# Optimization experiments

Measured on AMD Instinct MI355X. Metric: run time of the kernel, lower is better.

## Reference

```python
import jax, jax.numpy as jnp
import numpy as np

# ---- constants matching the original module's globals ----
H = 16          # self.h: number of bit levels; self.n = h per the source
TP = 8          # self.tp: parallel coordinate channels
N_K = 2         # random masks per flipped bit
T = 512         # T_train: tokens per block
N_TRNBR = 128   # neighbor count
K_VOCAB = 128   # sampled vocab count
N_VOCAB = 50257 # full vocab size V for sampled softmax correction
D = 256         # embedding dim
RATIO_COS = 1.0
RATIO_CRO = 0.1
C_CNC = 2 * H * N_K + 1  # candidate locations per token = 65


def setup_inputs() -> dict:
    key = jax.random.key(0)
    ks = jax.random.split(key, 8)
    n = H  # code: self.n = h
    sta_loc = jax.random.randint(ks[0], (T, TP), 1 - n, n, dtype=jnp.int32)
    nei_loc = jax.random.randint(ks[1], (T, N_TRNBR, TP), 1 - n, n, dtype=jnp.int32)
    voc_loc = jax.random.randint(ks[2], (T, K_VOCAB, TP), 1 - n, n, dtype=jnp.int32)
    sta_emb = jax.random.normal(ks[3], (T, D), dtype=jnp.float32)
    nei_emb = jax.random.normal(ks[4], (T, N_TRNBR, D), dtype=jnp.float32)
    voc_emb = jax.random.normal(ks[5], (T, K_VOCAB, D), dtype=jnp.float32)
    # raw random numbers for generate_random_masks: randint(0, self.n)
    rand_masks = jax.random.randint(ks[6], (T, H, N_K, TP), 0, n, dtype=jnp.int32)
    # converge mode: mask is all ones (generate_mask with converge=True)
    mask = jnp.ones((T, N_TRNBR), dtype=bool)
    return {"sta_loc": sta_loc, "nei_loc": nei_loc, "voc_loc": voc_loc,
            "sta_emb": sta_emb, "nei_emb": nei_emb, "voc_emb": voc_emb,
            "rand_masks": rand_masks, "mask": mask}


def _cos_similarity(c1, c2):
    # sign product: (+1 if >=0 else -1) for each operand
    sg = ((2 * (c1 >= 0).astype(jnp.int32) - 1) *
          (2 * (c2 >= 0).astype(jnp.int32) - 1)).astype(jnp.float32)
    x = ((jnp.abs(c1) ^ jnp.abs(c2)) + 1).astype(jnp.float32)
    # torch.frexp exponent of v>=1 equals floor(log2(v)) + 1
    expo = jnp.floor(jnp.log2(x)) + 1.0
    return sg * (1.0 - expo / H)


def _connection(sta_loc, rand_masks):
    bits = jnp.arange(H, dtype=jnp.int32)
    flip_masks = (1 << bits)                          # [H]
    flipped = sta_loc[:, None, :] ^ flip_masks[None, :, None]  # [T,H,TP]
    # note operator precedence in source: rn & (2**i - 1)
    rm = rand_masks & (flip_masks - 1)[None, :, None, None]    # [T,H,N_K,TP]
    res = (flipped[:, :, None, :] ^ rm).reshape(sta_loc.shape[0], H * N_K, TP)
    return jnp.concatenate([res, sta_loc[:, None, :], -res], axis=1)  # [T,C,TP]


def _normalize(x):
    return x / jnp.maximum(jnp.linalg.norm(x, axis=-1, keepdims=True), 1e-12)


def reference(sta_loc, nei_loc, voc_loc, sta_emb, nei_emb, voc_emb, rand_masks, mask):
    cnc_loc = _connection(sta_loc, rand_masks)          # [T, C, TP]
    lth = mask.sum(axis=1).astype(jnp.float32) + 1e-12  # [T]

    # euclidean-space cosine targets: [T, N_trnbr]
    eu_cos_val = jnp.einsum('td,tnd->tn', _normalize(sta_emb), _normalize(nei_emb))
    # use_eu_norm == True branch: ||sta|| * ||voc|| -> [T, K_vocab]
    eu_cro_nrm = (jnp.linalg.norm(sta_emb, axis=-1, keepdims=True) *
                  jnp.linalg.norm(voc_emb, axis=-1))

    pos_loc = jnp.concatenate([nei_loc, voc_loc], axis=1)           # [T, P, TP]
    cos_sta_pos = _cos_similarity(sta_loc[:, None, :], pos_loc)     # [T, P, TP]
    cos_sta_pos_sum = cos_sta_pos.sum(axis=-1)                      # [T, P]
    cos_cnc_pos = _cos_similarity(cnc_loc[:, None, :, :], pos_loc[:, :, None, :])  # [T,P,C,TP]
    ct_val = (cos_sta_pos_sum[:, :, None, None]
              - cos_sta_pos[:, :, None, :] + cos_cnc_pos) / TP      # [T,P,C,TP]

    # cosine-matching loss over neighbors
    eu = eu_cos_val[:, :, None, None]                               # [T,N,1,1]
    loss_cos = ((ct_val[:, :N_TRNBR] - eu) ** 2 * jnp.abs(eu)
                * mask[:, :, None, None].astype(jnp.float32))
    loss_cos = loss_cos.sum(axis=1) / lth[:, None, None]            # [T, C, TP]

    # sampled softmax CE (uniform proposal), positive class at vocab index 0
    z = ct_val[:, N_TRNBR:] * eu_cro_nrm[:, :, None, None]          # [T, K, C, TP]
    corr = jnp.where(jnp.arange(K_VOCAB) == 0, 0.0,
                     jnp.log(N_VOCAB / K_VOCAB)).astype(jnp.float32)
    zc = z + corr[None, :, None, None]
    loss_cro = jax.scipy.special.logsumexp(zc, axis=1) - zc[:, 0]   # [T, C, TP]

    loss_tot = RATIO_COS * loss_cos + RATIO_CRO * loss_cro

    # get_best_loc with cur_portion=1.0, cur_tp=tp -> pure argmin selection
    idx = jnp.argmin(loss_tot, axis=1)                              # [T, TP]
    gather = lambda a: jnp.take_along_axis(a, idx[:, None, :], axis=1)[:, 0]
    selected_locs = gather(cnc_loc)                                 # [T, TP]
    real_loss_cos = gather(loss_cos).mean(axis=-1)                  # [T]
    real_loss_cro = gather(loss_cro).mean(axis=-1)
    real_loss_tot = gather(loss_tot).mean(axis=-1)
    return selected_locs, real_loss_cos, real_loss_cro, real_loss_tot
```

## Files before the change

kernel.cpp:

```cpp
#include <hip/hip_runtime.h>
#include <math.h>

#define T_DIM 512
#define TP 8
#define NC 65
#define NJ 128
#define BLOCK 576
#define LOG2E 1.4426950408889634f
#define LN2   0.6931471805599453f
#define CORR_L2 8.617045f

__device__ __forceinline__ float i2f(int x) { return __int_as_float(x); }
__device__ __forceinline__ int   f2i(float x) { return __float_as_int(x); }

__device__ __forceinline__ int cand_v(int c, int sta, const int* s_rand, int p) {
    if (c == 32) return sta;
    const int cc = (c < 32) ? c : (c - 33);
    const int h = cc >> 1;
    const int r = (sta ^ (1 << h)) ^ (s_rand[cc * TP + p] & ((1 << h) - 1));
    return (c < 32) ? r : -r;
}

#define COS_STEP(va, vs, X, acc) do {                                   \
    const int _x = (va) ^ (X).x;                                        \
    const float _u8 = fmaf((float)__clz(_x + 1), 0.0078125f, -0.125f);  \
    const float _d = i2f(f2i(_u8) ^ ((vs) ^ (X).y)) + i2f((X).z);       \
    (acc) = fmaf(_d * _d, i2f((X).w), (acc));                           \
} while (0)

#define CRO_Z(va, vs, X) ({                                             \
    const int _x = (va) ^ (X).x;                                        \
    const float _u0 = fmaf((float)__clz(_x + 1), 0.0625f, -1.0f);       \
    const float _u = i2f(f2i(_u0) ^ ((vs) ^ (X).y));                    \
    fmaf(_u, i2f((X).w), i2f((X).z));                                   \
})

__device__ __forceinline__ float cos_body1(int va, int vs, const int4* pc) {
    float a0 = 0.f, a1 = 0.f;
    #pragma unroll 2
    for (int j = 0; j < NJ; j += 2) {
        const int4 x = pc[j * 8];
        const int4 y = pc[(j + 1) * 8];
        COS_STEP(va, vs, x, a0);
        COS_STEP(va, vs, y, a1);
    }
    return (a0 + a1) * 0.0078125f;
}

__device__ __forceinline__ void cos_body2(int vaA, int vsA, int vaB, int vsB,
                                          const int4* pc, float* oA, float* oB) {
    float a0 = 0.f, a1 = 0.f, b0 = 0.f, b1 = 0.f;
    #pragma unroll 2
    for (int j = 0; j < NJ; j += 2) {
        const int4 x = pc[j * 8];
        const int4 y = pc[(j + 1) * 8];
        COS_STEP(vaA, vsA, x, a0);
        COS_STEP(vaB, vsB, x, b0);
        COS_STEP(vaA, vsA, y, a1);
        COS_STEP(vaB, vsB, y, b1);
    }
    *oA = (a0 + a1) * 0.0078125f;
    *oB = (b0 + b1) * 0.0078125f;
}

__device__ __forceinline__ float cro_body1(int va, int vs, const int4* pc, float M) {
    const int4 x0 = pc[0];
    const float z0 = CRO_Z(va, vs, x0) - M;
    float s0 = __builtin_amdgcn_exp2f(z0);
    const int4 x1 = pc[8];
    float s1 = __builtin_amdgcn_exp2f(CRO_Z(va, vs, x1) - M);
    #pragma unroll 2
    for (int k = 2; k < NJ; k += 2) {
        const int4 x = pc[k * 8];
        const int4 y = pc[(k + 1) * 8];
        s0 += __builtin_amdgcn_exp2f(CRO_Z(va, vs, x) - M);
        s1 += __builtin_amdgcn_exp2f(CRO_Z(va, vs, y) - M);
    }
    const float S = fmaxf(s0 + s1, 1e-38f);
    return (__builtin_amdgcn_logf(S) - z0) * LN2;
}

__device__ __forceinline__ void cro_body2(int vaA, int vsA, int vaB, int vsB,
                                          const int4* pc, float M, float* oA, float* oB) {
    const int4 x0 = pc[0];
    const float zA0 = CRO_Z(vaA, vsA, x0) - M;
    const float zB0 = CRO_Z(vaB, vsB, x0) - M;
    float sA0 = __builtin_amdgcn_exp2f(zA0);
    float sB0 = __builtin_amdgcn_exp2f(zB0);
    const int4 x1 = pc[8];
    float sA1 = __builtin_amdgcn_exp2f(CRO_Z(vaA, vsA, x1) - M);
    float sB1 = __builtin_amdgcn_exp2f(CRO_Z(vaB, vsB, x1) - M);
    #pragma unroll 2
    for (int k = 2; k < NJ; k += 2) {
        const int4 x = pc[k * 8];
        const int4 y = pc[(k + 1) * 8];
        sA0 += __builtin_amdgcn_exp2f(CRO_Z(vaA, vsA, x) - M);
        sB0 += __builtin_amdgcn_exp2f(CRO_Z(vaB, vsB, x) - M);
        sA1 += __builtin_amdgcn_exp2f(CRO_Z(vaA, vsA, y) - M);
        sB1 += __builtin_amdgcn_exp2f(CRO_Z(vaB, vsB, y) - M);
    }
    const float SA = fmaxf(sA0 + sA1, 1e-38f);
    const float SB = fmaxf(sB0 + sB1, 1e-38f);
    *oA = (__builtin_amdgcn_logf(SA) - zA0) * LN2;
    *oB = (__builtin_amdgcn_logf(SB) - zB0) * LN2;
}

__global__ __launch_bounds__(BLOCK, 5) void cg_fused(
    const int* __restrict__ sta_loc,
    const int* __restrict__ nei_loc,
    const int* __restrict__ voc_loc,
    const float* __restrict__ sta_emb,
    const float* __restrict__ nei_emb,
    const float* __restrict__ voc_emb,
    const int* __restrict__ rand_masks,
    float* __restrict__ out)
{
    const int t = blockIdx.x;
    const int tid = threadIdx.x;

    __shared__ int4  s_pc4[2][NJ * TP];
    __shared__ float s_cspT[2][TP * 132];
    __shared__ float s_css[2][NJ];
    __shared__ float s_w[2][NJ];
    __shared__ float s_dot[NJ];
    __shared__ float s_nn[2][NJ];
    __shared__ float s_lcos[NC * TP], s_lcro[NC * TP];
    __shared__ float s_Mpart[9 * 8];
    __shared__ float s_ss;
    __shared__ int   s_sta[TP];
    __shared__ int   s_rand[256];

    if (tid < 256) s_rand[tid] = rand_masks[t * 256 + tid];

    if (tid < 512) {
        const int g = tid >> 2, sub = tid & 3;
        const float4* sp = (const float4*)(sta_emb + (size_t)t * 256);
        const float4* np = (const float4*)(nei_emb + ((size_t)t * NJ + g) * 256);
        const float4* vp = (const float4*)(voc_emb + ((size_t)t * NJ + g) * 256);
        float dd = 0.f, nnn = 0.f, nnv = 0.f, ss = 0.f;
        #pragma unroll 4
        for (int i = 0; i < 16; ++i) {
            const int i4 = sub + 4 * i;
            const float4 a = sp[i4];
            const float4 b = np[i4];
            const float4 c = vp[i4];
            dd  += a.x * b.x + a.y * b.y + a.z * b.z + a.w * b.w;
            nnn += b.x * b.x + b.y * b.y + b.z * b.z + b.w * b.w;
            nnv += c.x * c.x + c.y * c.y + c.z * c.z + c.w * c.w;
            if (g == 0) ss += a.x * a.x + a.y * a.y + a.z * a.z + a.w * a.w;
        }
        dd  += __shfl_xor(dd, 1);  dd  += __shfl_xor(dd, 2);
        nnn += __shfl_xor(nnn, 1); nnn += __shfl_xor(nnn, 2);
        nnv += __shfl_xor(nnv, 1); nnv += __shfl_xor(nnv, 2);
        if (g == 0) { ss += __shfl_xor(ss, 1); ss += __shfl_xor(ss, 2); }
        if (sub == 0) {
            s_dot[g] = dd; s_nn[0][g] = nnn; s_nn[1][g] = nnv;
            if (g == 0) s_ss = ss;
        }
    } else {
        const int l = tid - 512;
        if (l < TP) s_sta[l] = sta_loc[t * TP + l];
        const int4 sta4 = ((const int4*)(sta_loc + t * TP))[l & 1];
        const int sarr[4] = {sta4.x, sta4.y, sta4.z, sta4.w};
        #pragma unroll
        for (int side = 0; side < 2; ++side) {
            const int* loc = side ? voc_loc : nei_loc;
            const int4* lp = (const int4*)(loc + (size_t)t * 1024);
            #pragma unroll
            for (int q = 0; q < 4; ++q) {
                const int4 pl4 = lp[q * 64 + l];
                const int j = q * 32 + (l >> 1);
                const int parr[4] = {pl4.x, pl4.y, pl4.z, pl4.w};
                #pragma unroll
                for (int e = 0; e < 4; ++e) {
                    const int pl = parr[e];
                    const int sta = sarr[e];
                    const int idx = q * 256 + 4 * l + e;
                    const int qa = pl < 0 ? -pl : pl;
                    const int qsgn = pl & 0x80000000;
                    const int sa = sta < 0 ? -sta : sta;
                    const int x = sa ^ qa;
                    const float u0 = fmaf((float)__clz(x + 1), 0.0625f, -1.0f);
                    const float csp = i2f(f2i(u0) ^ ((sta ^ pl) & 0x80000000));
                    ((int2*)&s_pc4[side][idx])[0] = make_int2(qa, qsgn);
                    s_cspT[side][(4 * (l & 1) + e) * 132 + j] = csp;
                }
            }
        }
    }
    __syncthreads();

    if (tid < 256) {
        const int j = tid >> 1, side = tid & 1;
        float cs = 0.f;
        #pragma unroll
        for (int p = 0; p < TP; ++p) cs += s_cspT[side][p * 132 + j];
        s_css[side][j] = cs;
        const float ns = sqrtf(s_ss);
        const float nn = s_nn[side][j];
        if (side == 0)
            s_w[0][j] = s_dot[j] / (fmaxf(sqrtf(nn), 1e-12f) * fmaxf(ns, 1e-12f));
        else
            s_w[1][j] = ns * sqrtf(nn) * (0.125f * LOG2E);
    }
    __syncthreads();

    {
        float mloc = -INFINITY;
        #pragma unroll
        for (int k = 0; k < 4; ++k) {
            const int item = tid + k * BLOCK;
            if (item < 2048) {
                const int side = item >> 10, idx = item & 1023;
                const int j = idx >> 3, p = idx & 7;
                const float csp = s_cspT[side][p * 132 + j];
                const float b = s_css[side][j] - csp;
                const float w = s_w[side][j];
                float z2, w2;
                if (side == 0) { z2 = fmaf(b, 0.125f, -w); w2 = fabsf(w); }
                else {
                    z2 = fmaf(b, w, j ? CORR_L2 : 0.0f);
                    w2 = w;
                    mloc = fmaxf(mloc, z2 + w);
                }
                ((int2*)&s_pc4[side][idx])[1] = make_int2(f2i(z2), f2i(w2));
            }
        }
        mloc = fmaxf(mloc, __shfl_xor(mloc, 8));
        mloc = fmaxf(mloc, __shfl_xor(mloc, 16));
        mloc = fmaxf(mloc, __shfl_xor(mloc, 32));
        const int lane = tid & 63;
        if (lane < 8) s_Mpart[(tid >> 6) * 8 + lane] = mloc;
    }
    __syncthreads();

    if (tid < 256) {
        const int gk = tid >> 3, p = tid & 7;
        const int sta = s_sta[p];
        const int vA = cand_v(2 * gk, sta, s_rand, p);
        const int vB = cand_v(2 * gk + 1, sta, s_rand, p);
        cos_body2(vA < 0 ? -vA : vA, vA & 0x80000000,
                  vB < 0 ? -vB : vB, vB & 0x80000000, s_pc4[0] + p,
                  &s_lcos[(2 * gk) * TP + p], &s_lcos[(2 * gk + 1) * TP + p]);
    } else if (tid < 512) {
        const int w = tid - 256, gk = w >> 3, p = w & 7;
        const int sta = s_sta[p];
        const int vA = cand_v(2 * gk, sta, s_rand, p);
        const int vB = cand_v(2 * gk + 1, sta, s_rand, p);
        float M = s_Mpart[p];
        #pragma unroll
        for (int wv = 1; wv < 9; ++wv) M = fmaxf(M, s_Mpart[wv * 8 + p]);
        cro_body2(vA < 0 ? -vA : vA, vA & 0x80000000,
                  vB < 0 ? -vB : vB, vB & 0x80000000, s_pc4[1] + p, M,
                  &s_lcro[(2 * gk) * TP + p], &s_lcro[(2 * gk + 1) * TP + p]);
    } else if (tid < 520) {
        const int p = tid - 512;
        const int v = cand_v(64, s_sta[p], s_rand, p);
        s_lcos[64 * TP + p] =
            cos_body1(v < 0 ? -v : v, v & 0x80000000, s_pc4[0] + p);
    } else if (tid < 528) {
        const int p = tid - 520;
        const int v = cand_v(64, s_sta[p], s_rand, p);
        float M = s_Mpart[p];
        #pragma unroll
        for (int wv = 1; wv < 9; ++wv) M = fmaxf(M, s_Mpart[wv * 8 + p]);
        s_lcro[64 * TP + p] =
            cro_body1(v < 0 ? -v : v, v & 0x80000000, s_pc4[1] + p, M);
    }
    __syncthreads();

    float vc = 0.f, vr = 0.f, vt = 0.f;
    if (tid < TP) {
        const int p = tid;
        float best = INFINITY, blc = 0.f, blr = 0.f;
        int bc = 0;
        for (int c = 0; c < NC; ++c) {
            const float lc = s_lcos[c * TP + p];
            const float lr = s_lcro[c * TP + p];
            const float lt = fmaf(0.1f, lr, lc);
            if (lt < best) { best = lt; bc = c; blc = lc; blr = lr; }
        }
        out[t * TP + p] = (float)cand_v(bc, s_sta[p], s_rand, p);
        vc = blc; vr = blr; vt = best;
    }
    if (tid < 64) {
        vc += __shfl_xor(vc, 1); vc += __shfl_xor(vc, 2); vc += __shfl_xor(vc, 4);
        vr += __shfl_xor(vr, 1); vr += __shfl_xor(vr, 2); vr += __shfl_xor(vr, 4);
        vt += __shfl_xor(vt, 1); vt += __shfl_xor(vt, 2); vt += __shfl_xor(vt, 4);
        if (tid == 0) {
            out[T_DIM * TP + t] = vc * 0.125f;
            out[T_DIM * TP + T_DIM + t] = vr * 0.125f;
            out[T_DIM * TP + 2 * T_DIM + t] = vt * 0.125f;
        }
    }
}

extern "C" void kernel_launch(void* const* d_in, const int* in_sizes, int n_in,
                              void* d_out, int out_size, void* d_ws, size_t ws_size,
                              hipStream_t stream) {
    const int* sta_loc = (const int*)d_in[0];
    const int* nei_loc = (const int*)d_in[1];
    const int* voc_loc = (const int*)d_in[2];
    const float* sta_emb = (const float*)d_in[3];
    const float* nei_emb = (const float*)d_in[4];
    const float* voc_emb = (const float*)d_in[5];
    const int* rand_masks = (const int*)d_in[6];
    float* out = (float*)d_out;

    cg_fused<<<T_DIM, BLOCK, 0, stream>>>(
        sta_loc, nei_loc, voc_loc, sta_emb, nei_emb, voc_emb, rand_masks, out);
}
```

Baseline: 200.6 us.

## Split fused kernel into per-side blocks plus a combine kernel

Each token is now handled by two blocks, one for the neighbour/cosine side and one for the vocab/cross-entropy side, so 1024 blocks run instead of 512. The per-side losses go to a workspace, and a second small kernel does the argmin and averaging. This is meant to raise parallelism and cut the idle half of threads in the candidate phase, and it also removes one barrier by computing the row sums with a shuffle. The cost is a second launch and a global round trip through the workspace, and the sta_emb reads are duplicated across the two blocks.

```diff
diff --git a/kernel.cpp b/kernel.cpp
--- a/kernel.cpp
+++ b/kernel.cpp
@@ -9,6 +9,7 @@
 #define LOG2E 1.4426950408889634f
 #define LN2   0.6931471805599453f
 #define CORR_L2 8.617045f
+#define WSTRIDE (NC * TP)
 
 __device__ __forceinline__ float i2f(int x) { return __int_as_float(x); }
 __device__ __forceinline__ int   f2i(float x) { return __float_as_int(x); }
@@ -105,7 +106,7 @@
     *oB = (__builtin_amdgcn_logf(SB) - zB0) * LN2;
 }
 
-__global__ __launch_bounds__(BLOCK, 5) void cg_fused(
+__global__ __launch_bounds__(BLOCK, 5) void cg_side(
     const int* __restrict__ sta_loc,
     const int* __restrict__ nei_loc,
     const int* __restrict__ voc_loc,
@@ -113,18 +114,19 @@
     const float* __restrict__ nei_emb,
     const float* __restrict__ voc_emb,
     const int* __restrict__ rand_masks,
-    float* __restrict__ out)
+    float* __restrict__ wcos,
+    float* __restrict__ wcro)
 {
-    const int t = blockIdx.x;
+    const int bid = blockIdx.x;
+    const int side = bid & 1;
+    const int t = bid >> 1;
     const int tid = threadIdx.x;
 
-    __shared__ int4  s_pc4[2][NJ * TP];
-    __shared__ float s_cspT[2][TP * 132];
-    __shared__ float s_css[2][NJ];
-    __shared__ float s_w[2][NJ];
+    __shared__ int4  s_pc4[NJ * TP];
+    __shared__ float s_cspT[TP * 132];
+    __shared__ float s_css[NJ];
     __shared__ float s_dot[NJ];
-    __shared__ float s_nn[2][NJ];
-    __shared__ float s_lcos[NC * TP], s_lcro[NC * TP];
+    __shared__ float s_nn[NJ];
     __shared__ float s_Mpart[9 * 8];
     __shared__ float s_ss;
     __shared__ int   s_sta[TP];
@@ -135,26 +137,26 @@
     if (tid < 512) {
         const int g = tid >> 2, sub = tid & 3;
         const float4* sp = (const float4*)(sta_emb + (size_t)t * 256);
-        const float4* np = (const float4*)(nei_emb + ((size_t)t * NJ + g) * 256);
-        const float4* vp = (const float4*)(voc_emb + ((size_t)t * NJ + g) * 256);
-        float dd = 0.f, nnn = 0.f, nnv = 0.f, ss = 0.f;
+        const float* emb = side ? voc_emb : nei_emb;
+        const float4* ep = (const float4*)(emb + ((size_t)t * NJ + g) * 256);
+        float dd = 0.f, nn = 0.f, ss = 0.f;
         #pragma unroll 4
         for (int i = 0; i < 16; ++i) {
             const int i4 = sub + 4 * i;
-            const float4 a = sp[i4];
-            const float4 b = np[i4];
-            const float4 c = vp[i4];
-            dd  += a.x * b.x + a.y * b.y + a.z * b.z + a.w * b.w;
-            nnn += b.x * b.x + b.y * b.y + b.z * b.z + b.w * b.w;
-            nnv += c.x * c.x + c.y * c.y + c.z * c.z + c.w * c.w;
-            if (g == 0) ss += a.x * a.x + a.y * a.y + a.z * a.z + a.w * a.w;
-        }
-        dd  += __shfl_xor(dd, 1);  dd  += __shfl_xor(dd, 2);
-        nnn += __shfl_xor(nnn, 1); nnn += __shfl_xor(nnn, 2);
-        nnv += __shfl_xor(nnv, 1); nnv += __shfl_xor(nnv, 2);
+            const float4 b = ep[i4];
+            nn += b.x * b.x + b.y * b.y + b.z * b.z + b.w * b.w;
+            if (side == 0 || g == 0) {
+                const float4 a = sp[i4];
+                if (side == 0) dd += a.x * b.x + a.y * b.y + a.z * b.z + a.w * b.w;
+                if (g == 0)    ss += a.x * a.x + a.y * a.y + a.z * a.z + a.w * a.w;
+            }
+        }
+        nn += __shfl_xor(nn, 1); nn += __shfl_xor(nn, 2);
+        if (side == 0) { dd += __shfl_xor(dd, 1); dd += __shfl_xor(dd, 2); }
         if (g == 0) { ss += __shfl_xor(ss, 1); ss += __shfl_xor(ss, 2); }
         if (sub == 0) {
-            s_dot[g] = dd; s_nn[0][g] = nnn; s_nn[1][g] = nnv;
+            s_nn[g] = nn;
+            if (side == 0) s_dot[g] = dd;
             if (g == 0) s_ss = ss;
         }
     } else {
@@ -162,75 +164,67 @@
         if (l < TP) s_sta[l] = sta_loc[t * TP + l];
         const int4 sta4 = ((const int4*)(sta_loc + t * TP))[l & 1];
         const int sarr[4] = {sta4.x, sta4.y, sta4.z, sta4.w};
+        const int* loc = side ? voc_loc : nei_loc;
+        const int4* lp = (const int4*)(loc + (size_t)t * 1024);
         #pragma unroll
-        for (int side = 0; side < 2; ++side) {
-            const int* loc = side ? voc_loc : nei_loc;
-            const int4* lp = (const int4*)(loc + (size_t)t * 1024);
+        for (int q = 0; q < 4; ++q) {
+            const int4 pl4 = lp[q * 64 + l];
+            const int j = q * 32 + (l >> 1);
+            const int parr[4] = {pl4.x, pl4.y, pl4.z, pl4.w};
+            float cs4 = 0.f;
             #pragma unroll
-            for (int q = 0; q < 4; ++q) {
-                const int4 pl4 = lp[q * 64 + l];
-                const int j = q * 32 + (l >> 1);
-                const int parr[4] = {pl4.x, pl4.y, pl4.z, pl4.w};
-                #pragma unroll
-                for (int e = 0; e < 4; ++e) {
-                    const int pl = parr[e];
-                    const int sta = sarr[e];
-                    const int idx = q * 256 + 4 * l + e;
-                    const int qa = pl < 0 ? -pl : pl;
-                    const int qsgn = pl & 0x80000000;
-                    const int sa = sta < 0 ? -sta : sta;
-                    const int x = sa ^ qa;
-                    const float u0 = fmaf((float)__clz(x + 1), 0.0625f, -1.0f);
-                    const float csp = i2f(f2i(u0) ^ ((sta ^ pl) & 0x80000000));
-                    ((int2*)&s_pc4[side][idx])[0] = make_int2(qa, qsgn);
-                    s_cspT[side][(4 * (l & 1) + e) * 132 + j] = csp;
-                }
+            for (int e = 0; e < 4; ++e) {
+                const int pl = parr[e];
+                const int sta = sarr[e];
+                const int idx = q * 256 + 4 * l + e;
+                const int qa = pl < 0 ? -pl : pl;
+                const int qsgn = pl & 0x80000000;
+                const int sa = sta < 0 ? -sta : sta;
+                const int x = sa ^ qa;
+                const float u0 = fmaf((float)__clz(x + 1), 0.0625f, -1.0f);
+                const float csp = i2f(f2i(u0) ^ ((sta ^ pl) & 0x80000000));
+                ((int2*)&s_pc4[idx])[0] = make_int2(qa, qsgn);
+                s_cspT[(4 * (l & 1) + e) * 132 + j] = csp;
+                cs4 += csp;
             }
+            const float cs8 = cs4 + __shfl_xor(cs4, 1);
+            if (!(l & 1)) s_css[j] = cs8;
         }
     }
     __syncthreads();
 
-    if (tid < 256) {
-        const int j = tid >> 1, side = tid & 1;
-        float cs = 0.f;
-        #pragma unroll
-        for (int p = 0; p < TP; ++p) cs += s_cspT[side][p * 132 + j];
-        s_css[side][j] = cs;
+    {
         const float ns = sqrtf(s_ss);
-        const float nn = s_nn[side][j];
-        if (side == 0)
-            s_w[0][j] = s_dot[j] / (fmaxf(sqrtf(nn), 1e-12f) * fmaxf(ns, 1e-12f));
-        else
-            s_w[1][j] = ns * sqrtf(nn) * (0.125f * LOG2E);
-    }
-    __syncthreads();
-
-    {
         float mloc = -INFINITY;
         #pragma unroll
-        for (int k = 0; k < 4; ++k) {
+        for (int k = 0; k < 2; ++k) {
             const int item = tid + k * BLOCK;
-            if (item < 2048) {
-                const int side = item >> 10, idx = item & 1023;
-                const int j = idx >> 3, p = idx & 7;
-                const float csp = s_cspT[side][p * 132 + j];
-                const float b = s_css[side][j] - csp;
-                const float w = s_w[side][j];
+            if (item < 1024) {
+                const int j = item >> 3;
+                const int p = item & 7;
+                const float csp = s_cspT[p * 132 + j];
+                const float b = s_css[j] - csp;
                 float z2, w2;
-                if (side == 0) { z2 = fmaf(b, 0.125f, -w); w2 = fabsf(w); }
-                else {
-                    z2 = fmaf(b, w, j ? CORR_L2 : 0.0f);
-                    w2 = w;
-                    mloc = fmaxf(mloc, z2 + w);
+                if (side == 0) {
+                    const float w = s_dot[j] /
+                        (fmaxf(sqrtf(s_nn[j]), 1e-12f) * fmaxf(ns, 1e-12f));
+                    z2 = fmaf(b, 0.125f, -w); w2 = fabsf(w);
+                } else {
+                    const float A = ns * sqrtf(s_nn[j]) * (0.125f * LOG2E);
+                    z2 = fmaf(b, A, j ? CORR_L2 : 0.0f);
+                    w2 = A;
+                    mloc = fmaxf(mloc, z2 + A);
                 }
-                ((int2*)&s_pc4[side][idx])[1] = make_int2(f2i(z2), f2i(w2));
+                ((int2*)&s_pc4[item])[1] = make_int2(f2i(z2), f2i(w2));
             }
         }
-        mloc = fmaxf(mloc, __shfl_xor(mloc, 8));
-        mloc = fmaxf(mloc, __shfl_xor(mloc, 16));
-        mloc = fmaxf(mloc, __shfl_xor(mloc, 32));
-        const int lane = tid & 63;
-        if (lane < 8) s_Mpart[(tid >> 6) * 8 + lane] = mloc;
+        if (side) {
+            mloc = fmaxf(mloc, __shfl_xor(mloc, 8));
+            mloc = fmaxf(mloc, __shfl_xor(mloc, 16));
+            mloc = fmaxf(mloc, __shfl_xor(mloc, 32));
+            const int lane = tid & 63;
+            if (lane < 8) s_Mpart[(tid >> 6) * 8 + lane] = mloc;
+        }
     }
     __syncthreads();
 
@@ -239,59 +233,80 @@
         const int sta = s_sta[p];
         const int vA = cand_v(2 * gk, sta, s_rand, p);
         const int vB = cand_v(2 * gk + 1, sta, s_rand, p);
-        cos_body2(vA < 0 ? -vA : vA, vA & 0x80000000,
-                  vB < 0 ? -vB : vB, vB & 0x80000000, s_pc4[0] + p,
-                  &s_lcos[(2 * gk) * TP + p], &s_lcos[(2 * gk + 1) * TP + p]);
-    } else if (tid < 512) {
-        const int w = tid - 256, gk = w >> 3, p = w & 7;
-        const int sta = s_sta[p];
-        const int vA = cand_v(2 * gk, sta, s_rand, p);
-        const int vB = cand_v(2 * gk + 1, sta, s_rand, p);
-        float M = s_Mpart[p];
-        #pragma unroll
-        for (int wv = 1; wv < 9; ++wv) M = fmaxf(M, s_Mpart[wv * 8 + p]);
-        cro_body2(vA < 0 ? -vA : vA, vA & 0x80000000,
-                  vB < 0 ? -vB : vB, vB & 0x80000000, s_pc4[1] + p, M,
-                  &s_lcro[(2 * gk) * TP + p], &s_lcro[(2 * gk + 1) * TP + p]);
-    } else if (tid < 520) {
-        const int p = tid - 512;
+        float oA, oB;
+        if (side == 0) {
+            cos_body2(vA < 0 ? -vA : vA, vA & 0x80000000,
+                      vB < 0 ? -vB : vB, vB & 0x80000000, s_pc4 + p, &oA, &oB);
+            wcos[t * WSTRIDE + (2 * gk) * TP + p] = oA;
+            wcos[t * WSTRIDE + (2 * gk + 1) * TP + p] = oB;
+        } else {
+            float M = s_Mpart[p];
+            #pragma unroll
+            for (int wv = 1; wv < 9; ++wv) M = fmaxf(M, s_Mpart[wv * 8 + p]);
+            cro_body2(vA < 0 ? -vA : vA, vA & 0x80000000,
+                      vB < 0 ? -vB : vB, vB & 0x80000000, s_pc4 + p, M, &oA, &oB);
+            wcro[t * WSTRIDE + (2 * gk) * TP + p] = oA;
+            wcro[t * WSTRIDE + (2 * gk + 1) * TP + p] = oB;
+        }
+    } else if (tid < 264) {
+        const int p = tid - 256;
         const int v = cand_v(64, s_sta[p], s_rand, p);
-        s_lcos[64 * TP + p] =
-            cos_body1(v < 0 ? -v : v, v & 0x80000000, s_pc4[0] + p);
-    } else if (tid < 528) {
-        const int p = tid - 520;
-        const int v = cand_v(64, s_sta[p], s_rand, p);
-        float M = s_Mpart[p];
-        #pragma unroll
-        for (int wv = 1; wv < 9; ++wv) M = fmaxf(M, s_Mpart[wv * 8 + p]);
-        s_lcro[64 * TP + p] =
-            cro_body1(v < 0 ? -v : v, v & 0x80000000, s_pc4[1] + p, M);
-    }
-    __syncthreads();
+        if (side == 0) {
+            wcos[t * WSTRIDE + 64 * TP + p] =
+                cos_body1(v < 0 ? -v : v, v & 0x80000000, s_pc4 + p);
+        } else {
+            float M = s_Mpart[p];
+            #pragma unroll
+            for (int wv = 1; wv < 9; ++wv) M = fmaxf(M, s_Mpart[wv * 8 + p]);
+            wcro[t * WSTRIDE + 64 * TP + p] =
+                cro_body1(v < 0 ? -v : v, v & 0x80000000, s_pc4 + p, M);
+        }
+    }
+}
+
+__global__ void cg_combine(
+    const int* __restrict__ sta_loc,
+    const int* __restrict__ rand_masks,
+    const float* __restrict__ wcos,
+    const float* __restrict__ wcro,
+    float* __restrict__ out)
+{
+    const int t = blockIdx.x;
+    const int tid = threadIdx.x;
+    const int p = tid & 7, cg = tid >> 3;
+
+    float best = INFINITY, blc = 0.f, blr = 0.f;
+    int bc = NC;
+    for (int c = cg; c < NC; c += 8) {
+        const float lc = wcos[t * WSTRIDE + c * TP + p];
+        const float lr = wcro[t * WSTRIDE + c * TP + p];
+        const float lt = fmaf(0.1f, lr, lc);
+        if (lt < best) { best = lt; bc = c; blc = lc; blr = lr; }
+    }
+    #pragma unroll
+    for (int d = 8; d < 64; d <<= 1) {
+        const float o_best = __shfl_xor(best, d);
+        const float o_blc  = __shfl_xor(blc, d);
+        const float o_blr  = __shfl_xor(blr, d);
+        const int   o_bc   = __shfl_xor(bc, d);
+        if (o_best < best || (o_best == best && o_bc < bc)) {
+            best = o_best; bc = o_bc; blc = o_blc; blr = o_blr;
+        }
+    }
 
     float vc = 0.f, vr = 0.f, vt = 0.f;
     if (tid < TP) {
-        const int p = tid;
-        float best = INFINITY, blc = 0.f, blr = 0.f;
-        int bc = 0;
-        for (int c = 0; c < NC; ++c) {
-            const float lc = s_lcos[c * TP + p];
-            const float lr = s_lcro[c * TP + p];
-            const float lt = fmaf(0.1f, lr, lc);
-            if (lt < best) { best = lt; bc = c; blc = lc; blr = lr; }
-        }
-        out[t * TP + p] = (float)cand_v(bc, s_sta[p], s_rand, p);
+        const int sta = sta_loc[t * TP + tid];
+        out[t * TP + tid] = (float)cand_v(bc, sta, rand_masks + t * 256, tid);
         vc = blc; vr = blr; vt = best;
     }
-    if (tid < 64) {
-        vc += __shfl_xor(vc, 1); vc += __shfl_xor(vc, 2); vc += __shfl_xor(vc, 4);
-        vr += __shfl_xor(vr, 1); vr += __shfl_xor(vr, 2); vr += __shfl_xor(vr, 4);
-        vt += __shfl_xor(vt, 1); vt += __shfl_xor(vt, 2); vt += __shfl_xor(vt, 4);
-        if (tid == 0) {
-            out[T_DIM * TP + t] = vc * 0.125f;
-            out[T_DIM * TP + T_DIM + t] = vr * 0.125f;
-            out[T_DIM * TP + 2 * T_DIM + t] = vt * 0.125f;
-        }
+    vc += __shfl_xor(vc, 1); vc += __shfl_xor(vc, 2); vc += __shfl_xor(vc, 4);
+    vr += __shfl_xor(vr, 1); vr += __shfl_xor(vr, 2); vr += __shfl_xor(vr, 4);
+    vt += __shfl_xor(vt, 1); vt += __shfl_xor(vt, 2); vt += __shfl_xor(vt, 4);
+    if (tid == 0) {
+        out[T_DIM * TP + t] = vc * 0.125f;
+        out[T_DIM * TP + T_DIM + t] = vr * 0.125f;
+        out[T_DIM * TP + 2 * T_DIM + t] = vt * 0.125f;
     }
 }
 
@@ -307,6 +322,11 @@
     const int* rand_masks = (const int*)d_in[6];
     float* out = (float*)d_out;
 
-    cg_fused<<<T_DIM, BLOCK, 0, stream>>>(
-        sta_loc, nei_loc, voc_loc, sta_emb, nei_emb, voc_emb, rand_masks, out);
-}
+    float* wcos = (float*)d_ws;
+    float* wcro = wcos + (size_t)WSTRIDE * T_DIM;
+
+    cg_side<<<2 * T_DIM, BLOCK, 0, stream>>>(
+        sta_loc, nei_loc, voc_loc, sta_emb, nei_emb, voc_emb, rand_masks,
+        wcos, wcro);
+    cg_combine<<<T_DIM, 64, 0, stream>>>(sta_loc, rand_masks, wcos, wcro, out);
+}
```

Result: faster. 188.8 us (-5.9%).
